# Optimization experiments

Hardware: AMD Instinct MI355X
Metric: run time of the kernel (lower is better)

## Reference

```python
import jax, jax.numpy as jnp
import numpy as np

N_NODES = 200000
N_EDGES = 1600000
N_GRAPHS = 2000
IN_DIM, W1_DIM, W2_DIM, N_CLASSES = 8, 64, 12, 2


def setup_inputs() -> dict:
    key = jax.random.key(0)
    ks = jax.random.split(key, 9)
    x = jax.random.normal(ks[0], (N_NODES, IN_DIM), dtype=jnp.float32)
    edge_index = jax.random.randint(ks[1], (2, N_EDGES), 0, N_NODES, dtype=jnp.int64)
    batch_index = jnp.sort(jax.random.randint(ks[2], (N_NODES,), 0, N_GRAPHS, dtype=jnp.int64))
    # Glorot-ish scaled params
    W1 = jax.random.normal(ks[3], (IN_DIM, W1_DIM), dtype=jnp.float32) * (1.0 / np.sqrt(IN_DIM))
    b1 = jnp.zeros((W1_DIM,), dtype=jnp.float32)
    W2 = jax.random.normal(ks[4], (W1_DIM, W2_DIM), dtype=jnp.float32) * (1.0 / np.sqrt(W1_DIM))
    b2 = jnp.zeros((W2_DIM,), dtype=jnp.float32)
    Wl = jax.random.normal(ks[5], (W2_DIM, N_CLASSES), dtype=jnp.float32) * (1.0 / np.sqrt(W2_DIM))
    bl = jnp.zeros((N_CLASSES,), dtype=jnp.float32)
    return {"x": x, "edge_index": edge_index, "batch_index": batch_index,
            "W1": W1, "b1": b1, "W2": W2, "b2": b2, "Wl": Wl, "bl": bl}


def _gcn_conv(x, W, b, src, dst, deg_inv_sqrt, n_nodes):
    # x' = D^{-1/2} (A + I) D^{-1/2} X W + b  (self-loops already in src/dst)
    xw = x @ W                                   # [N, out]
    norm = deg_inv_sqrt[src] * deg_inv_sqrt[dst]  # [E+N]
    msg = xw[src] * norm[:, None]                 # edge-wise gather (memory-bound)
    out = jax.ops.segment_sum(msg, dst, num_segments=n_nodes)
    return out + b


def reference(x, edge_index, batch_index, W1, b1, W2, b2, Wl, bl):
    n = x.shape[0]
    loops = jnp.arange(n, dtype=edge_index.dtype)
    src = jnp.concatenate([edge_index[0], loops])
    dst = jnp.concatenate([edge_index[1], loops])
    # degree (with self-loops) on destination nodes, as in PyG gcn_norm
    deg = jax.ops.segment_sum(jnp.ones_like(dst, dtype=x.dtype), dst, num_segments=n)
    deg_inv_sqrt = jax.lax.rsqrt(deg)  # deg >= 1 due to self-loops
    h = jax.nn.relu(_gcn_conv(x, W1, b1, src, dst, deg_inv_sqrt, n))
    h = jax.nn.relu(_gcn_conv(h, W2, b2, src, dst, deg_inv_sqrt, n))
    pooled = jax.ops.segment_max(h, batch_index, num_segments=N_GRAPHS)  # global_max_pool
    logits = pooled @ Wl + bl
    return jax.nn.log_softmax(logits, axis=1)
```

## Files before the change

kernel.cpp:

```cpp
#include <hip/hip_runtime.h>
#include <hip/hip_fp16.h>
#include <stdint.h>


constexpr int IN_DIM = 8;
constexpr int H1 = 64;
constexpr int H2 = 12;
constexpr int NPB = 256;
constexpr int NBK = 782;
constexpr int CAP = 2560;
constexpr int CHUNK = 4096;
constexpr int SLOTS = 16;

__device__ __forceinline__ void acc_row8(float* acc, int4 rv) {
    const __half2* h = (const __half2*)&rv;
#pragma unroll
    for (int q = 0; q < 4; ++q) {
        float2 f = __half22float2(h[q]);
        acc[2 * q] += f.x; acc[2 * q + 1] += f.y;
    }
}

__global__ void __launch_bounds__(256) k_binA(
        const int* __restrict__ src, const int* __restrict__ dst,
        uint32_t* __restrict__ pairs, int* __restrict__ bcursor, int ne) {
    __shared__ int s_cnt[NBK];
    __shared__ int s_start[NBK];
    __shared__ int s_gb[NBK];
    __shared__ int s_tmp[256];
    __shared__ uint32_t s_img[CHUNK];
    __shared__ uint16_t s_bkt[CHUNK];
    int t = threadIdx.x;
    for (int i = t; i < NBK; i += 256) s_cnt[i] = 0;
    __syncthreads();
    int e0 = blockIdx.x * CHUNK;
    int cntblk = min(CHUNK, ne - e0);
    int rec[16];
#pragma unroll
    for (int i = 0; i < 16; ++i) {
        int e = e0 + i * 256 + t;
        rec[i] = -1;
        if (e < ne) {
            int d = __builtin_nontemporal_load(&dst[e]);
            int b = d >> 8;
            int off = atomicAdd(&s_cnt[b], 1);
            rec[i] = (off << 18) | ((d & 255) << 10) | b;
        }
    }
    __syncthreads();
    int b4 = t * 4;
    int v0 = (b4 < NBK) ? s_cnt[b4] : 0;
    int v1 = (b4 + 1 < NBK) ? s_cnt[b4 + 1] : 0;
    int v2 = (b4 + 2 < NBK) ? s_cnt[b4 + 2] : 0;
    int v3 = (b4 + 3 < NBK) ? s_cnt[b4 + 3] : 0;
    int p1 = v0, p2 = v0 + v1, p3 = v0 + v1 + v2, tot = p3 + v3;
    s_tmp[t] = tot;
    __syncthreads();
    for (int off = 1; off < 256; off <<= 1) {
        int u = (t >= off) ? s_tmp[t - off] : 0;
        __syncthreads();
        s_tmp[t] += u;
        __syncthreads();
    }
    int ex = s_tmp[t] - tot;
    if (b4 < NBK)     s_start[b4] = ex;
    if (b4 + 1 < NBK) s_start[b4 + 1] = ex + p1;
    if (b4 + 2 < NBK) s_start[b4 + 2] = ex + p2;
    if (b4 + 3 < NBK) s_start[b4 + 3] = ex + p3;
    for (int b = t; b < NBK; b += 256) {
        int c = s_cnt[b];
        s_gb[b] = (c > 0) ? atomicAdd(&bcursor[b], c) : 0;
    }
    __syncthreads();
#pragma unroll
    for (int i = 0; i < 16; ++i) {
        if (rec[i] < 0) continue;
        int e = e0 + i * 256 + t;
        int b = rec[i] & 1023;
        int dl = (rec[i] >> 10) & 255;
        int off = rec[i] >> 18;
        int pos = s_start[b] + off;
        s_img[pos] = ((uint32_t)dl << 18) | (uint32_t)__builtin_nontemporal_load(&src[e]);
        s_bkt[pos] = (uint16_t)b;
    }
    __syncthreads();
    for (int i = t; i < cntblk; i += 256) {
        int b = s_bkt[i];
        int goff = s_gb[b] + (i - s_start[b]);
        if (goff < CAP) pairs[(size_t)b * CAP + goff] = s_img[i];
    }
}

__global__ void __launch_bounds__(256) k_binB(
        const uint32_t* __restrict__ pairs, const int* __restrict__ bcursor,
        const float* __restrict__ x, int* __restrict__ csr_pad,
        int* __restrict__ csr_ovf, unsigned int* __restrict__ meta,
        float* __restrict__ dis, __half2* __restrict__ xdh, int n) {
    __shared__ int s_hist[NPB];
    __shared__ int s_start[NPB];
    __shared__ int s_cur[NPB];
    __shared__ int s_tmp[256];
    __shared__ int s_pad[NPB * SLOTS];
    int b = blockIdx.x;
    int t = threadIdx.x;
    int cnt = min(bcursor[b], CAP);
    const uint32_t* pb = pairs + (size_t)b * CAP;
    s_hist[t] = 0; s_cur[t] = 0;
    for (int i = t; i < NPB * SLOTS; i += 256) s_pad[i] = n;
    __syncthreads();
    for (int i = t; i < cnt; i += 256)
        atomicAdd(&s_hist[__builtin_nontemporal_load(&pb[i]) >> 18], 1);
    __syncthreads();
    int v = s_hist[t];
    s_tmp[t] = v;
    __syncthreads();
    for (int off = 1; off < 256; off <<= 1) {
        int u = (t >= off) ? s_tmp[t - off] : 0;
        __syncthreads();
        s_tmp[t] += u;
        __syncthreads();
    }
    s_start[t] = s_tmp[t] - v;
    __syncthreads();
    int cb = b * CAP;
    int node = (b << 8) + t;
    if (node < n) {
        int deg = s_hist[t];
        meta[node] = ((unsigned int)deg << 21) | (unsigned int)(cb + s_start[t]);
        float di = rsqrtf((float)(deg + 1));
        dis[node] = di;
        const float4* xi = (const float4*)(x + (size_t)node * IN_DIM);
        float4 a = xi[0], c = xi[1];
        union { __half2 h[4]; int iv[4]; } u;
        u.h[0] = __float22half2_rn(make_float2(a.x * di, a.y * di));
        u.h[1] = __float22half2_rn(make_float2(a.z * di, a.w * di));
        u.h[2] = __float22half2_rn(make_float2(c.x * di, c.y * di));
        u.h[3] = __float22half2_rn(make_float2(c.z * di, c.w * di));
        ((int4*)xdh)[node] = make_int4(u.iv[0], u.iv[1], u.iv[2], u.iv[3]);
    } else if (node == n) {
        ((int4*)xdh)[n] = make_int4(0, 0, 0, 0);
    }
    __syncthreads();
    for (int i = t; i < cnt; i += 256) {
        uint32_t p = __builtin_nontemporal_load(&pb[i]);
        int dl = p >> 18;
        int sidx = (int)(p & 0x3FFFFu);
        int pos = atomicAdd(&s_cur[dl], 1);
        if (pos < SLOTS) s_pad[dl * SLOTS + pos] = sidx;
        else             csr_ovf[cb + s_start[dl] + pos] = sidx;
    }
    __syncthreads();
    for (int i = t; i < NPB * SLOTS / 4; i += 256) {
        int node2 = (b << 8) + (i >> 2);
        if (node2 < n)
            ((int4*)csr_pad)[(size_t)(b << 8) * 4 + i] = ((int4*)s_pad)[i];
    }
}

__global__ void __launch_bounds__(256) k_agg1f(
        const int* __restrict__ csr_pad, const int* __restrict__ csr_ovf,
        const unsigned int* __restrict__ meta, const __half2* __restrict__ xdh,
        const float* __restrict__ dis, const float* __restrict__ W1,
        const float* __restrict__ b1, const float* __restrict__ W2,
        __half2* __restrict__ y2h, int n) {
    __shared__ float sW1[IN_DIM * H1];
    __shared__ float sW2[H1 * H2];
    __shared__ float sb1[H1];
    for (int i = threadIdx.x; i < IN_DIM * H1; i += 256) sW1[i] = W1[i];
    for (int i = threadIdx.x; i < H1 * H2; i += 256) sW2[i] = W2[i];
    if (threadIdx.x < H1) sb1[threadIdx.x] = b1[threadIdx.x];
    __syncthreads();
    int node = blockIdx.x * 256 + threadIdx.x;
    if (node > n) return;
    int4* orow = (int4*)y2h + (size_t)node * 2;
    if (node == n) {
        orow[0] = make_int4(0, 0, 0, 0);
        orow[1] = make_int4(0, 0, 0, 0);
        return;
    }
    const int4* pr = (const int4*)(csr_pad + (size_t)node * SLOTS);
    int4 p0 = pr[0], p1 = pr[1], p2 = pr[2], p3 = pr[3];
    unsigned int m = meta[node];
    const int4* xt = (const int4*)xdh;

    float acc[8] = {0, 0, 0, 0, 0, 0, 0, 0};
    int idx[16] = {p0.x, p0.y, p0.z, p0.w, p1.x, p1.y, p1.z, p1.w,
                   p2.x, p2.y, p2.z, p2.w, p3.x, p3.y, p3.z, p3.w};
    acc_row8(acc, xt[node]);
#pragma unroll
    for (int i = 0; i < 16; ++i) acc_row8(acc, xt[(size_t)idx[i]]);
    int deg = m >> 21;
    if (deg > SLOTS) {
        int r0 = (int)(m & 0x1FFFFF);
        for (int r = SLOTS; r < deg; ++r) acc_row8(acc, xt[(size_t)csr_ovf[r0 + r]]);
    }
    float di = dis[node];
    float z[8];
#pragma unroll
    for (int k = 0; k < 8; ++k) z[k] = acc[k] * di;

    float y2[H2];
#pragma unroll
    for (int j = 0; j < H2; ++j) y2[j] = 0.f;
    for (int d = 0; d < H1; ++d) {
        float h = sb1[d];
#pragma unroll
        for (int k = 0; k < 8; ++k) h = fmaf(z[k], sW1[k * H1 + d], h);
        h = fmaxf(h, 0.f);
#pragma unroll
        for (int j = 0; j < H2; ++j) y2[j] = fmaf(h, sW2[d * H2 + j], y2[j]);
    }
    union { __half2 h2v[8]; int iv[8]; } u;
#pragma unroll
    for (int q = 0; q < 6; ++q)
        u.h2v[q] = __float22half2_rn(make_float2(y2[2 * q] * di, y2[2 * q + 1] * di));
    u.h2v[6] = __float22half2_rn(make_float2(0.f, 0.f));
    u.h2v[7] = u.h2v[6];
    orow[0] = make_int4(u.iv[0], u.iv[1], u.iv[2], u.iv[3]);
    orow[1] = make_int4(u.iv[4], u.iv[5], u.iv[6], u.iv[7]);
}

__global__ void __launch_bounds__(256) k_agg2(
        const int* __restrict__ csr_pad, const int* __restrict__ csr_ovf,
        const unsigned int* __restrict__ meta, const __half2* __restrict__ y2h,
        const float* __restrict__ dis, const float* __restrict__ b2,
        const int* __restrict__ batch, unsigned int* __restrict__ pooled, int n) {
    int node = blockIdx.x * 256 + threadIdx.x;
    int lane = threadIdx.x & 63;
    bool active = node < n;
    float v[12] = {0, 0, 0, 0, 0, 0, 0, 0, 0, 0, 0, 0};
    int gid = 0x7fffffff;
    if (active) {
        const int4* pr = (const int4*)(csr_pad + (size_t)node * SLOTS);
        int4 p0 = pr[0], p1 = pr[1], p2 = pr[2], p3 = pr[3];
        unsigned int m = meta[node];
        const int4* yt = (const int4*)y2h;
        float acc[12] = {0, 0, 0, 0, 0, 0, 0, 0, 0, 0, 0, 0};
        auto addrow = [&](int nb) {
            int4 ra = yt[(size_t)nb * 2];
            int4 rb = yt[(size_t)nb * 2 + 1];
            const __half2* ha = (const __half2*)&ra;
            const __half2* hb = (const __half2*)&rb;
#pragma unroll
            for (int q = 0; q < 4; ++q) {
                float2 f = __half22float2(ha[q]);
                acc[2 * q] += f.x; acc[2 * q + 1] += f.y;
            }
#pragma unroll
            for (int q = 0; q < 2; ++q) {
                float2 f = __half22float2(hb[q]);
                acc[8 + 2 * q] += f.x; acc[9 + 2 * q] += f.y;
            }
        };
        int idx[16] = {p0.x, p0.y, p0.z, p0.w, p1.x, p1.y, p1.z, p1.w,
                       p2.x, p2.y, p2.z, p2.w, p3.x, p3.y, p3.z, p3.w};
        addrow(node);
#pragma unroll
        for (int i = 0; i < 16; ++i) addrow(idx[i]);
        int deg = m >> 21;
        if (deg > SLOTS) {
            int r0 = (int)(m & 0x1FFFFF);
            for (int r = SLOTS; r < deg; ++r) addrow(csr_ovf[r0 + r]);
        }
        float di = dis[node];
#pragma unroll
        for (int q = 0; q < 12; ++q) v[q] = fmaxf(fmaf(acc[q], di, b2[q]), 0.f);
        gid = batch[node];
    }
#pragma unroll
    for (int off = 1; off < 64; off <<= 1) {
        int g2 = __shfl_up(gid, off, 64);
        bool merge = (lane >= off) && (g2 == gid);
#pragma unroll
        for (int q = 0; q < 12; ++q) {
            float tv = __shfl_up(v[q], off, 64);
            if (merge) v[q] = fmaxf(v[q], tv);
        }
    }
    int gnext = __shfl_down(gid, 1, 64);
    bool last = (lane == 63) || (gnext != gid);
    if (last && gid != 0x7fffffff) {
        unsigned int* pp = pooled + (size_t)gid * 12;
#pragma unroll
        for (int q = 0; q < 12; ++q) atomicMax(&pp[q], __float_as_uint(v[q]));
    }
}

__global__ void k_head(const unsigned int* __restrict__ pooled,
                       const float* __restrict__ Wl, const float* __restrict__ bl,
                       float* __restrict__ out, int g) {
    int i = blockIdx.x * 256 + threadIdx.x;
    if (i >= g) return;
    float l0 = bl[0], l1 = bl[1];
#pragma unroll
    for (int k = 0; k < H2; ++k) {
        float pv = __uint_as_float(pooled[(size_t)i * 12 + k]);
        l0 = fmaf(pv, Wl[k * 2 + 0], l0);
        l1 = fmaf(pv, Wl[k * 2 + 1], l1);
    }
    float m = fmaxf(l0, l1);
    float lse = m + logf(expf(l0 - m) + expf(l1 - m));
    out[i * 2 + 0] = l0 - lse;
    out[i * 2 + 1] = l1 - lse;
}

extern "C" void kernel_launch(void* const* d_in, const int* in_sizes, int n_in,
                              void* d_out, int out_size, void* d_ws, size_t ws_size,
                              hipStream_t stream) {
    const float* x   = (const float*)d_in[0];
    const int* ei    = (const int*)d_in[1];
    const int* batch = (const int*)d_in[2];
    const float* W1  = (const float*)d_in[3];
    const float* b1  = (const float*)d_in[4];
    const float* W2  = (const float*)d_in[5];
    const float* b2  = (const float*)d_in[6];
    const float* Wl  = (const float*)d_in[7];
    const float* bl  = (const float*)d_in[8];
    float* out = (float*)d_out;

    const int N = in_sizes[0] / IN_DIM;
    const int E = in_sizes[1] / 2;
    const int G = out_size / 2;
    const int* src = ei;
    const int* dst = ei + E;

    auto cdiv = [](long long a, int b) { return (int)((a + b - 1) / b); };

    char* wp = (char*)d_ws;
    auto carve = [&](size_t bytes) {
        char* p = wp;
        wp += (bytes + 63) & ~(size_t)63;
        return p;
    };
    int*          bcursor = (int*)carve(NBK * 4);
    unsigned int* pooled  = (unsigned int*)carve((size_t)G * H2 * 4);
    unsigned int* meta    = (unsigned int*)carve((size_t)N * 4);
    float*        dis     = (float*)carve((size_t)N * 4);
    __half2*      xdh     = (__half2*)carve((size_t)(N + 1) * 16);
    __half2*      y2h     = (__half2*)carve((size_t)(N + 1) * 32);
    uint32_t*     pairs   = (uint32_t*)carve((size_t)NBK * CAP * 4);
    int*          csr_pad = (int*)carve((size_t)N * SLOTS * 4);
    int*          csr_ovf = (int*)carve((size_t)NBK * CAP * 4);

    size_t zspan = (char*)(pooled + (size_t)G * H2) - (char*)bcursor;
    (void)hipMemsetAsync(bcursor, 0, zspan, stream);

    k_binA<<<cdiv(E, CHUNK), 256, 0, stream>>>(src, dst, pairs, bcursor, E);
    k_binB<<<NBK, 256, 0, stream>>>(pairs, bcursor, x, csr_pad, csr_ovf,
                                    meta, dis, xdh, N);

    k_agg1f<<<cdiv((long long)N + 1, 256), 256, 0, stream>>>(
        csr_pad, csr_ovf, meta, xdh, dis, W1, b1, W2, y2h, N);
    k_agg2<<<cdiv(N, 256), 256, 0, stream>>>(csr_pad, csr_ovf, meta, y2h, dis, b2,
                                             batch, pooled, N);
    k_head<<<cdiv(G, 256), 256, 0, stream>>>(pooled, Wl, bl, out, G);
}
```

Baseline: 175.2 us.

## Split layer-2 features into 16B and 8B planes and aggregate in two passes

The layer-2 intermediate, previously stored as a 32-byte padded fp16 row, is split into an 8-channel 16-byte array and a 4-channel 8-byte array, with two aggregation kernels each gathering one plane. This removes the padding bytes and keeps each gather table small so it fits better in cache during random neighbor access. In exchange, the CSR indices, meta and batch arrays are read twice and there is an extra kernel launch.

```diff
diff --git a/kernel.cpp b/kernel.cpp
--- a/kernel.cpp
+++ b/kernel.cpp
@@ -16,6 +16,14 @@
     const __half2* h = (const __half2*)&rv;
 #pragma unroll
     for (int q = 0; q < 4; ++q) {
+        float2 f = __half22float2(h[q]);
+        acc[2 * q] += f.x; acc[2 * q + 1] += f.y;
+    }
+}
+__device__ __forceinline__ void acc_row4(float* acc, int2 rv) {
+    const __half2* h = (const __half2*)&rv;
+#pragma unroll
+    for (int q = 0; q < 2; ++q) {
         float2 f = __half22float2(h[q]);
         acc[2 * q] += f.x; acc[2 * q + 1] += f.y;
     }
@@ -162,7 +170,7 @@
         const unsigned int* __restrict__ meta, const __half2* __restrict__ xdh,
         const float* __restrict__ dis, const float* __restrict__ W1,
         const float* __restrict__ b1, const float* __restrict__ W2,
-        __half2* __restrict__ y2h, int n) {
+        __half2* __restrict__ y2a, __half2* __restrict__ y2b, int n) {
     __shared__ float sW1[IN_DIM * H1];
     __shared__ float sW2[H1 * H2];
     __shared__ float sb1[H1];
@@ -172,10 +180,9 @@
     __syncthreads();
     int node = blockIdx.x * 256 + threadIdx.x;
     if (node > n) return;
-    int4* orow = (int4*)y2h + (size_t)node * 2;
     if (node == n) {
-        orow[0] = make_int4(0, 0, 0, 0);
-        orow[1] = make_int4(0, 0, 0, 0);
+        ((int4*)y2a)[n] = make_int4(0, 0, 0, 0);
+        ((int2*)y2b)[n] = make_int2(0, 0);
         return;
     }
     const int4* pr = (const int4*)(csr_pad + (size_t)node * SLOTS);
@@ -210,61 +217,47 @@
 #pragma unroll
         for (int j = 0; j < H2; ++j) y2[j] = fmaf(h, sW2[d * H2 + j], y2[j]);
     }
-    union { __half2 h2v[8]; int iv[8]; } u;
-#pragma unroll
-    for (int q = 0; q < 6; ++q)
-        u.h2v[q] = __float22half2_rn(make_float2(y2[2 * q] * di, y2[2 * q + 1] * di));
-    u.h2v[6] = __float22half2_rn(make_float2(0.f, 0.f));
-    u.h2v[7] = u.h2v[6];
-    orow[0] = make_int4(u.iv[0], u.iv[1], u.iv[2], u.iv[3]);
-    orow[1] = make_int4(u.iv[4], u.iv[5], u.iv[6], u.iv[7]);
-}
-
-__global__ void __launch_bounds__(256) k_agg2(
+    union { __half2 h2v[4]; int iv[4]; } ua;
+#pragma unroll
+    for (int q = 0; q < 4; ++q)
+        ua.h2v[q] = __float22half2_rn(make_float2(y2[2 * q] * di, y2[2 * q + 1] * di));
+    ((int4*)y2a)[node] = make_int4(ua.iv[0], ua.iv[1], ua.iv[2], ua.iv[3]);
+    union { __half2 h2v[2]; int iv[2]; } ub;
+#pragma unroll
+    for (int q = 0; q < 2; ++q)
+        ub.h2v[q] = __float22half2_rn(make_float2(y2[8 + 2 * q] * di, y2[9 + 2 * q] * di));
+    ((int2*)y2b)[node] = make_int2(ub.iv[0], ub.iv[1]);
+}
+
+__global__ void __launch_bounds__(256) k_agg2a(
         const int* __restrict__ csr_pad, const int* __restrict__ csr_ovf,
-        const unsigned int* __restrict__ meta, const __half2* __restrict__ y2h,
+        const unsigned int* __restrict__ meta, const __half2* __restrict__ y2a,
         const float* __restrict__ dis, const float* __restrict__ b2,
         const int* __restrict__ batch, unsigned int* __restrict__ pooled, int n) {
     int node = blockIdx.x * 256 + threadIdx.x;
     int lane = threadIdx.x & 63;
     bool active = node < n;
-    float v[12] = {0, 0, 0, 0, 0, 0, 0, 0, 0, 0, 0, 0};
+    float v[8] = {0, 0, 0, 0, 0, 0, 0, 0};
     int gid = 0x7fffffff;
     if (active) {
         const int4* pr = (const int4*)(csr_pad + (size_t)node * SLOTS);
         int4 p0 = pr[0], p1 = pr[1], p2 = pr[2], p3 = pr[3];
         unsigned int m = meta[node];
-        const int4* yt = (const int4*)y2h;
-        float acc[12] = {0, 0, 0, 0, 0, 0, 0, 0, 0, 0, 0, 0};
-        auto addrow = [&](int nb) {
-            int4 ra = yt[(size_t)nb * 2];
-            int4 rb = yt[(size_t)nb * 2 + 1];
-            const __half2* ha = (const __half2*)&ra;
-            const __half2* hb = (const __half2*)&rb;
-#pragma unroll
-            for (int q = 0; q < 4; ++q) {
-                float2 f = __half22float2(ha[q]);
-                acc[2 * q] += f.x; acc[2 * q + 1] += f.y;
-            }
-#pragma unroll
-            for (int q = 0; q < 2; ++q) {
-                float2 f = __half22float2(hb[q]);
-                acc[8 + 2 * q] += f.x; acc[9 + 2 * q] += f.y;
-            }
-        };
+        const int4* yt = (const int4*)y2a;
+        float acc[8] = {0, 0, 0, 0, 0, 0, 0, 0};
         int idx[16] = {p0.x, p0.y, p0.z, p0.w, p1.x, p1.y, p1.z, p1.w,
                        p2.x, p2.y, p2.z, p2.w, p3.x, p3.y, p3.z, p3.w};
-        addrow(node);
-#pragma unroll
-        for (int i = 0; i < 16; ++i) addrow(idx[i]);
+        acc_row8(acc, yt[node]);
+#pragma unroll
+        for (int i = 0; i < 16; ++i) acc_row8(acc, yt[(size_t)idx[i]]);
         int deg = m >> 21;
         if (deg > SLOTS) {
             int r0 = (int)(m & 0x1FFFFF);
-            for (int r = SLOTS; r < deg; ++r) addrow(csr_ovf[r0 + r]);
+            for (int r = SLOTS; r < deg; ++r) acc_row8(acc, yt[(size_t)csr_ovf[r0 + r]]);
         }
         float di = dis[node];
 #pragma unroll
-        for (int q = 0; q < 12; ++q) v[q] = fmaxf(fmaf(acc[q], di, b2[q]), 0.f);
+        for (int q = 0; q < 8; ++q) v[q] = fmaxf(fmaf(acc[q], di, b2[q]), 0.f);
         gid = batch[node];
     }
 #pragma unroll
@@ -272,7 +265,7 @@
         int g2 = __shfl_up(gid, off, 64);
         bool merge = (lane >= off) && (g2 == gid);
 #pragma unroll
-        for (int q = 0; q < 12; ++q) {
+        for (int q = 0; q < 8; ++q) {
             float tv = __shfl_up(v[q], off, 64);
             if (merge) v[q] = fmaxf(v[q], tv);
         }
@@ -282,7 +275,57 @@
     if (last && gid != 0x7fffffff) {
         unsigned int* pp = pooled + (size_t)gid * 12;
 #pragma unroll
-        for (int q = 0; q < 12; ++q) atomicMax(&pp[q], __float_as_uint(v[q]));
+        for (int q = 0; q < 8; ++q) atomicMax(&pp[q], __float_as_uint(v[q]));
+    }
+}
+
+__global__ void __launch_bounds__(256) k_agg2b(
+        const int* __restrict__ csr_pad, const int* __restrict__ csr_ovf,
+        const unsigned int* __restrict__ meta, const __half2* __restrict__ y2b,
+        const float* __restrict__ dis, const float* __restrict__ b2,
+        const int* __restrict__ batch, unsigned int* __restrict__ pooled, int n) {
+    int node = blockIdx.x * 256 + threadIdx.x;
+    int lane = threadIdx.x & 63;
+    bool active = node < n;
+    float v[4] = {0, 0, 0, 0};
+    int gid = 0x7fffffff;
+    if (active) {
+        const int4* pr = (const int4*)(csr_pad + (size_t)node * SLOTS);
+        int4 p0 = pr[0], p1 = pr[1], p2 = pr[2], p3 = pr[3];
+        unsigned int m = meta[node];
+        const int2* yt = (const int2*)y2b;
+        float acc[4] = {0, 0, 0, 0};
+        int idx[16] = {p0.x, p0.y, p0.z, p0.w, p1.x, p1.y, p1.z, p1.w,
+                       p2.x, p2.y, p2.z, p2.w, p3.x, p3.y, p3.z, p3.w};
+        acc_row4(acc, yt[node]);
+#pragma unroll
+        for (int i = 0; i < 16; ++i) acc_row4(acc, yt[(size_t)idx[i]]);
+        int deg = m >> 21;
+        if (deg > SLOTS) {
+            int r0 = (int)(m & 0x1FFFFF);
+            for (int r = SLOTS; r < deg; ++r) acc_row4(acc, yt[(size_t)csr_ovf[r0 + r]]);
+        }
+        float di = dis[node];
+#pragma unroll
+        for (int q = 0; q < 4; ++q) v[q] = fmaxf(fmaf(acc[q], di, b2[8 + q]), 0.f);
+        gid = batch[node];
+    }
+#pragma unroll
+    for (int off = 1; off < 64; off <<= 1) {
+        int g2 = __shfl_up(gid, off, 64);
+        bool merge = (lane >= off) && (g2 == gid);
+#pragma unroll
+        for (int q = 0; q < 4; ++q) {
+            float tv = __shfl_up(v[q], off, 64);
+            if (merge) v[q] = fmaxf(v[q], tv);
+        }
+    }
+    int gnext = __shfl_down(gid, 1, 64);
+    bool last = (lane == 63) || (gnext != gid);
+    if (last && gid != 0x7fffffff) {
+        unsigned int* pp = pooled + (size_t)gid * 12;
+#pragma unroll
+        for (int q = 0; q < 4; ++q) atomicMax(&pp[8 + q], __float_as_uint(v[q]));
     }
 }
 
@@ -337,7 +380,8 @@
     unsigned int* meta    = (unsigned int*)carve((size_t)N * 4);
     float*        dis     = (float*)carve((size_t)N * 4);
     __half2*      xdh     = (__half2*)carve((size_t)(N + 1) * 16);
-    __half2*      y2h     = (__half2*)carve((size_t)(N + 1) * 32);
+    __half2*      y2a     = (__half2*)carve((size_t)(N + 1) * 16);
+    __half2*      y2b     = (__half2*)carve((size_t)(N + 1) * 8);
     uint32_t*     pairs   = (uint32_t*)carve((size_t)NBK * CAP * 4);
     int*          csr_pad = (int*)carve((size_t)N * SLOTS * 4);
     int*          csr_ovf = (int*)carve((size_t)NBK * CAP * 4);
@@ -350,8 +394,10 @@
                                     meta, dis, xdh, N);
 
     k_agg1f<<<cdiv((long long)N + 1, 256), 256, 0, stream>>>(
-        csr_pad, csr_ovf, meta, xdh, dis, W1, b1, W2, y2h, N);
-    k_agg2<<<cdiv(N, 256), 256, 0, stream>>>(csr_pad, csr_ovf, meta, y2h, dis, b2,
-                                             batch, pooled, N);
+        csr_pad, csr_ovf, meta, xdh, dis, W1, b1, W2, y2a, y2b, N);
+    k_agg2a<<<cdiv(N, 256), 256, 0, stream>>>(csr_pad, csr_ovf, meta, y2a, dis, b2,
+                                              batch, pooled, N);
+    k_agg2b<<<cdiv(N, 256), 256, 0, stream>>>(csr_pad, csr_ovf, meta, y2b, dis, b2,
+                                              batch, pooled, N);
     k_head<<<cdiv(G, 256), 256, 0, stream>>>(pooled, Wl, bl, out, G);
 }
```

Result: slower. 180.3 us (+2.9%).
